# Optimization experiments

Hardware: AMD Instinct MI355X
Metric: run time of the kernel (lower is better)

Reference implementation:

```python
import jax, jax.numpy as jnp
import numpy as np

B, G, A = 16, 50, 81920          # batch, max_gt_num, anchor_num
T, P = 128, 64                   # train_anchors_num, max positives (T*positive_ratios)
NNEG = T - P                     # max negatives per image
BIG = 1e10


def setup_inputs():
    key = jax.random.key(0)
    k1, k2, k3, k4, k5, k6, k7 = jax.random.split(key, 7)
    # anchors: CTPN-style, fixed width 16, heights ~[11, 273]
    ay1 = jax.random.uniform(k1, (B, A)) * 960.0
    ax1 = jax.random.uniform(k2, (B, A)) * 1000.0
    ah = jax.random.uniform(k3, (B, A)) * 262.0 + 11.0
    anchors = jnp.stack([ay1, ax1, ay1 + ah, ax1 + 16.0], axis=-1)
    # gt boxes: 30 valid per image, rest padding (tag=0)
    gy1 = jax.random.uniform(k4, (B, G)) * 900.0
    gx1 = jax.random.uniform(k5, (B, G)) * 600.0
    gh = jax.random.uniform(k6, (B, G)) * 180.0 + 20.0
    gw = jax.random.uniform(k7, (B, G)) * 380.0 + 16.0
    tag = jnp.broadcast_to((jnp.arange(G) < 30).astype(jnp.float32), (B, G))
    boxes = jnp.stack([gy1, gx1, gy1 + gh, gx1 + gw], axis=-1) * tag[..., None]
    gt_boxes = jnp.concatenate([boxes, tag[..., None]], axis=-1)       # [B,G,5]
    gt_cls = jnp.stack([tag, tag], axis=-1)                            # [B,G,2] (class_id, tag)
    valid_anchors_indices = jnp.broadcast_to(jnp.arange(A, dtype=jnp.int32), (B, A))
    return {"gt_boxes": gt_boxes, "gt_cls": gt_cls, "anchors": anchors,
            "valid_anchors_indices": valid_anchors_indices}


def _compute_iou(gb, an):
    # gb [G,4], an [A,4] -> [G,A]
    iw = jnp.maximum(0.0, jnp.minimum(gb[:, None, 3], an[None, :, 3]) -
                     jnp.maximum(gb[:, None, 1], an[None, :, 1]))
    ih = jnp.maximum(0.0, jnp.minimum(gb[:, None, 2], an[None, :, 2]) -
                     jnp.maximum(gb[:, None, 0], an[None, :, 0]))
    inter = iw * ih
    area_g = (gb[:, 3] - gb[:, 1]) * (gb[:, 2] - gb[:, 0])
    area_a = (an[:, 3] - an[:, 1]) * (an[:, 2] - an[:, 0])
    return inter / (area_g[:, None] + area_a[None, :] - inter)


def _one_image(gt_boxes, gt_cls, anchors, valid_idx, key):
    gt_tag = gt_boxes[:, 4] > 0                       # [G] padding mask
    gb = gt_boxes[:, :4]
    gcls = gt_cls[:, 0]
    gt_num = jnp.sum(gt_tag.astype(jnp.float32))

    iou = _compute_iou(gb, anchors) * gt_tag[:, None].astype(jnp.float32)   # [G,A]
    gt_max_bool = (iou == jnp.max(iou, axis=1, keepdims=True)) & gt_tag[:, None]
    a_max = jnp.max(iou, axis=0, keepdims=True)
    a_thr = jnp.where(a_max >= 0.7, a_max, 1.0)
    pos_mat = (gt_max_bool | (iou == a_thr)) & gt_tag[:, None]              # [G,A]

    k1, k2 = jax.random.split(key)
    # --- positive sampling (random shuffle -> random-score top_k) ---
    flat = pos_mat.reshape(-1)
    score = jnp.where(flat, jax.random.uniform(k1, (G * A,)), -1.0)
    top_s, top_i = jax.lax.top_k(score, P)
    pos_valid = top_s >= 0.0                                               # [P]
    pos_num = jnp.sum(pos_valid.astype(jnp.int32))
    gt_i = top_i // A
    a_i = top_i % A
    pa = anchors[a_i]
    pg = gb[gt_i]
    pc = gcls[gt_i] * pos_valid
    h = pa[:, 2] - pa[:, 0]
    gt_h = jnp.where(pos_valid, pg[:, 2] - pg[:, 0], h)   # safe for padding slots
    dy = ((pg[:, 2] + pg[:, 0]) - (pa[:, 2] + pa[:, 0])) * 0.5 / h
    dh = jnp.log(gt_h / h)
    pd = jnp.stack([dy / 0.1, dh / 0.2], axis=1) * pos_valid[:, None]       # [P,2]

    # --- side anchors per gt ---
    x1b = jnp.broadcast_to(anchors[:, 1][None, :], (G, A))
    left_i = jnp.argmin(jnp.where(pos_mat, x1b, BIG), axis=1)
    right_i = jnp.argmax(jnp.where(pos_mat, x1b, -BIG), axis=1)
    la, ra = anchors[left_i], anchors[right_i]
    ld = (gb[:, 1] - (la[:, 3] + la[:, 1]) * 0.5) / (la[:, 3] - la[:, 1]) / 0.1
    rd = (gb[:, 3] - (ra[:, 3] + ra[:, 1]) * 0.5) / (ra[:, 3] - ra[:, 1]) / 0.1
    gtf = gt_tag.astype(jnp.float32)
    side_deltas = jnp.stack([ld * gtf, rd * gtf, gtf], axis=1)              # [G,3]
    gti = gt_tag.astype(jnp.int32)
    side_indices = jnp.stack([valid_idx[left_i] * gti, valid_idx[right_i] * gti, gti], axis=1)

    # --- negative sampling ---
    neg_bool = (jnp.max(iou, axis=0) < 0.5) & ~jnp.any(pos_mat, axis=0)
    nscore = jnp.where(neg_bool, jax.random.uniform(k2, (A,)), -1.0)
    ns, ni = jax.lax.top_k(nscore, NNEG)
    neg_avail = jnp.sum((ns >= 0.0).astype(jnp.int32))
    neg_num = jnp.minimum(jnp.minimum(NNEG, T - pos_num), neg_avail)

    # --- fixed-size assembly: slots [0,pos_num)=pos, [pos_num,pos_num+neg_num)=neg ---
    i = jnp.arange(T)
    is_pos = i < pos_num
    is_neg = (i >= pos_num) & (i < pos_num + neg_num)
    pi = jnp.clip(i, 0, P - 1)
    nj = jnp.clip(i - pos_num, 0, NNEG - 1)
    tagc = (is_pos | is_neg).astype(jnp.float32)
    deltas = jnp.concatenate([jnp.where(is_pos[:, None], pd[pi], 0.0), tagc[:, None]], axis=1)
    class_ids = jnp.stack([jnp.where(is_pos, pc[pi], 0.0), tagc], axis=1)
    idx_pos = valid_idx[a_i]                                                # [P]
    ind = jnp.where(is_pos, idx_pos[pi],
                    jnp.where(is_neg, ni[nj].astype(jnp.int32), 0))
    ind_tag = jnp.where(is_pos, 1, jnp.where(is_neg, -1, 0)).astype(jnp.int32)
    indices = jnp.stack([ind, ind_tag], axis=1)

    return (deltas, class_ids, indices, side_deltas, side_indices,
            gt_num, pos_num.astype(jnp.float32), neg_num.astype(jnp.float32))


def reference(gt_boxes, gt_cls, anchors, valid_anchors_indices):
    keys = jax.random.split(jax.random.key(42), B)
    return jax.vmap(_one_image)(gt_boxes, gt_cls, anchors, valid_anchors_indices, keys)
```

## Files before the change

kernel.cpp:

```cpp
#include <hip/hip_runtime.h>
#include <stdint.h>

namespace ct {
constexpr int B = 16, G = 50, A = 81920, T = 128;
constexpr int NB2 = 64;
constexpr int CH2 = A / (NB2 * 256);
constexpr int CAPP = 16384;
constexpr int CAPN = 16384;
constexpr int STG  = 7168;
constexpr int NX = 16, NY = 20, NCELL = NX * NY;
constexpr float NEG_T1 = 0.992f;

constexpr size_t O_DELTAS = 0;
constexpr size_t O_CLS = O_DELTAS + (size_t)B * T * 3;
constexpr size_t O_IND = O_CLS + (size_t)B * T * 2;
constexpr size_t O_SD  = O_IND + (size_t)B * T * 2;
constexpr size_t O_SI  = O_SD + (size_t)B * G * 3;
constexpr size_t O_GTN = O_SI + (size_t)B * G * 3;
constexpr size_t O_PN  = O_GTN + B;
constexpr size_t O_NN  = O_PN + B;

constexpr size_t W_KEYS  = 0;
constexpr size_t W_GTMAX = 256;
constexpr size_t W_LEFT  = 4096;
constexpr size_t W_RIGHT = 10496;
constexpr size_t W_CPOS  = 17408;
constexpr size_t W_CT1   = 18432;
constexpr size_t W_PNN   = 19456;
constexpr size_t W_BCNT  = 19584;
constexpr size_t W_PD0   = 24064;
constexpr size_t W_PD1   = W_PD0 + 4ull * B * 64;
constexpr size_t W_PC    = W_PD1 + 4ull * B * 64;
constexpr size_t W_IPF   = W_PC  + 4ull * B * 64;
constexpr size_t W_NI    = W_IPF + 4ull * B * 64;
constexpr size_t W_POSL  = W_NI  + 4ull * B * 64;
constexpr size_t W_NT1   = W_POSL + 8ull * B * CAPP;
constexpr size_t W_CMASK = W_NT1  + 8ull * B * CAPN;
}

struct U2 { uint32_t x, y; };

__device__ __forceinline__ U2 threefry(uint32_t k0, uint32_t k1, uint32_t x0, uint32_t x1) {
  uint32_t ks2 = k0 ^ k1 ^ 0x1BD11BDAu;
  x0 += k0; x1 += k1;
#define TFR(r) { x0 += x1; x1 = (x1 << (r)) | (x1 >> (32 - (r))); x1 ^= x0; }
  TFR(13) TFR(15) TFR(26) TFR(6)  x0 += k1;  x1 += ks2 + 1u;
  TFR(17) TFR(29) TFR(16) TFR(24) x0 += ks2; x1 += k0 + 2u;
  TFR(13) TFR(15) TFR(26) TFR(6)  x0 += k0;  x1 += k1 + 3u;
  TFR(17) TFR(29) TFR(16) TFR(24) x0 += k1;  x1 += ks2 + 4u;
  TFR(13) TFR(15) TFR(26) TFR(6)  x0 += ks2; x1 += k0 + 5u;
#undef TFR
  return {x0, x1};
}

__device__ __forceinline__ uint32_t rnd_bits(uint32_t ka, uint32_t kb, uint32_t idx) {
  U2 o = threefry(ka, kb, 0u, idx);
  return o.x ^ o.y;
}

__device__ __forceinline__ void iou_parts(float g0, float g1, float g2, float g3,
                                          float garea,
                                          float a0, float a1, float a2, float a3,
                                          float aarea, float& inter, float& denom) {
#pragma clang fp contract(off)
  float iw = fminf(g3, a3) - fmaxf(g1, a1);
  iw = fmaxf(0.0f, iw);
  float ih = fminf(g2, a2) - fmaxf(g0, a0);
  ih = fmaxf(0.0f, ih);
  inter = iw * ih;
  denom = (garea + aarea) - inter;
}

__device__ __forceinline__ void compact_gts(const float* gt_boxes, int b, int tid,
                                            float4* sgA, float* sgG, int* sgO,
                                            int* sn) {
  using namespace ct;
  int lane = tid & 63;
  if (tid < 64) {
    bool pred = false;
    float g0 = 0, g1 = 0, g2 = 0, g3 = 0;
    if (tid < G) {
      const float* gp = gt_boxes + ((size_t)b * G + tid) * 5;
      g0 = gp[0]; g1 = gp[1]; g2 = gp[2]; g3 = gp[3];
      pred = gp[4] > 0.0f;
    }
    unsigned long long mk = __ballot(pred);
    int slot = (int)__popcll(mk & ((1ull << lane) - 1ull));
    if (pred) {
      sgA[slot] = make_float4(g0, g1, g2, g3);
      sgG[slot] = (g3 - g1) * (g2 - g0);
      sgO[slot] = tid;
    }
    if (lane == 0) *sn = (int)__popcll(mk);
  }
}

__global__ __launch_bounds__(256) void k01_init(const float* __restrict__ gt_boxes,
                                                char* ws) {
  using namespace ct;
  __shared__ float4 sgA[64];
  __shared__ float  sgG[64];
  __shared__ int    sgO[64];
  __shared__ int    sn;
  int b = blockIdx.x, tid = threadIdx.x;
  if (tid == 0) {
    uint32_t* keys = (uint32_t*)(ws + W_KEYS);
    U2 kb = threefry(0u, 42u, 0u, (uint32_t)b);
    U2 s0 = threefry(kb.x, kb.y, 0u, 0u);
    U2 s1 = threefry(kb.x, kb.y, 0u, 1u);
    keys[b * 4 + 0] = s0.x; keys[b * 4 + 1] = s0.y;
    keys[b * 4 + 2] = s1.x; keys[b * 4 + 3] = s1.y;
    ((uint32_t*)(ws + W_CPOS))[b * 16] = 0u;
    ((uint32_t*)(ws + W_CT1))[b * 16] = 0u;
    ((uint32_t*)(ws + W_PNN))[b] = 0u;
    ((uint32_t*)(ws + W_PNN))[16 + b] = 0u;
  }
  if (tid >= 64 && tid < 64 + G) {
    int i = tid - 64;
    ((unsigned long long*)(ws + W_LEFT))[(size_t)b * G + i] = ~0ull;
    ((unsigned long long*)(ws + W_RIGHT))[(size_t)b * G + i] = 0ull;
    ((uint32_t*)(ws + W_GTMAX))[(size_t)b * G + i] = 0u;
  }
  compact_gts(gt_boxes, b, tid, sgA, sgG, sgO, &sn);
  __syncthreads();
  int ntag = sn;
  unsigned long long* cm = (unsigned long long*)(ws + W_CMASK) + (size_t)b * NCELL;
  for (int c = tid; c < NCELL; c += 256) {
    int cx = c & (NX - 1), cy = c >> 4;
    float x0 = cx * 64.0f, x1 = x0 + 64.0f;
    float y0 = cy * 64.0f, y1 = y0 + 64.0f;
    unsigned long long m = 0;
    for (int j = 0; j < ntag; ++j) {
      float4 g = sgA[j];
      if (g.y < x1 && g.w > x0 && g.x < y1 && g.z > y0) m |= 1ull << j;
    }
    cm[c] = m;
  }
}

__device__ __forceinline__ unsigned long long anchor_mask(const unsigned long long* sCM,
                                                          float4 an) {
  using namespace ct;
  int cx0 = min((int)an.y >> 6, NX - 1), cx1 = min((int)an.w >> 6, NX - 1);
  int cy0 = min((int)an.x >> 6, NY - 1), cy1 = min((int)an.z >> 6, NY - 1);
  unsigned long long mask = 0;
  for (int cy = cy0; cy <= cy1; ++cy)
    for (int cx = cx0; cx <= cx1; ++cx)
      mask |= sCM[cy * NX + cx];
  return mask;
}

__global__ __launch_bounds__(256) void k1b_gtmax(const float* __restrict__ anchors,
                                                 const float* __restrict__ gt_boxes,
                                                 char* ws) {
  using namespace ct;
  __shared__ float4 sgA[64];
  __shared__ float  sgG[64];
  __shared__ int    sgO[64];
  __shared__ int    sn;
  __shared__ uint32_t sGm[64];
  __shared__ unsigned long long sCM[NCELL];
  int b = blockIdx.y, tid = threadIdx.x;
  compact_gts(gt_boxes, b, tid, sgA, sgG, sgO, &sn);
  if (tid < 64) sGm[tid] = 0u;
  const unsigned long long* cm = (const unsigned long long*)(ws + W_CMASK) + (size_t)b * NCELL;
  for (int c = tid; c < NCELL; c += 256) sCM[c] = cm[c];
  __syncthreads();
  const float4* ap = (const float4*)(anchors + (size_t)b * A * 4);
  for (int c = 0; c < CH2; ++c) {
    int a = (blockIdx.x * CH2 + c) * 256 + tid;
    float4 an = ap[a];
    float aarea = (an.w - an.y) * (an.z - an.x);
    unsigned long long mask = anchor_mask(sCM, an);
    while (mask) {
      int j = (int)(__ffsll((long long)mask) - 1);
      mask &= mask - 1;
      float4 g = sgA[j];
      float inter, denom;
      iou_parts(g.x, g.y, g.z, g.w, sgG[j], an.x, an.y, an.z, an.w, aarea, inter, denom);
      float v = inter / denom;
      if (v > 0.0f) atomicMax(&sGm[j], __float_as_uint(v));
    }
  }
  __syncthreads();
  if (tid < sn && sGm[tid] != 0u)
    atomicMax((uint32_t*)(ws + W_GTMAX) + (size_t)b * G + sgO[tid], sGm[tid]);
}

__global__ __launch_bounds__(256) void k2_posneg(const float* __restrict__ anchors,
                                                 const float* __restrict__ gt_boxes,
                                                 char* ws) {
  using namespace ct;
  __shared__ float4 sgA[64];
  __shared__ float  sgG[64];
  __shared__ int    sgO[64];
  __shared__ float  sgM[64];
  __shared__ int    sn;
  __shared__ unsigned long long sCM[NCELL];
  __shared__ uint32_t sT1C[CH2];
  __shared__ uint32_t sWT1[CH2][4];
  __shared__ uint32_t sPfx[CH2];
  __shared__ uint32_t sNegW[4];
  __shared__ uint32_t sT1Base;
  int b = blockIdx.y, tid = threadIdx.x, lane = tid & 63, wid = tid >> 6;
  compact_gts(gt_boxes, b, tid, sgA, sgG, sgO, &sn);
  if (tid < CH2) sT1C[tid] = 0u;
  const unsigned long long* cm = (const unsigned long long*)(ws + W_CMASK) + (size_t)b * NCELL;
  for (int c = tid; c < NCELL; c += 256) sCM[c] = cm[c];
  __syncthreads();
  if (tid < sn)
    sgM[tid] = __uint_as_float(((const uint32_t*)(ws + W_GTMAX))[(size_t)b * G + sgO[tid]]);
  __syncthreads();

  const uint32_t* keys = (const uint32_t*)(ws + W_KEYS);
  uint32_t k1a = keys[b * 4 + 0], k1b = keys[b * 4 + 1];
  uint32_t k2a = keys[b * 4 + 2], k2b = keys[b * 4 + 3];
  unsigned long long* posl  = (unsigned long long*)(ws + W_POSL) + (size_t)b * CAPP;
  unsigned long long* negt1 = (unsigned long long*)(ws + W_NT1)  + (size_t)b * CAPN;
  unsigned long long* left  = (unsigned long long*)(ws + W_LEFT)  + (size_t)b * G;
  unsigned long long* right = (unsigned long long*)(ws + W_RIGHT) + (size_t)b * G;
  const float4* ap = (const float4*)(anchors + (size_t)b * A * 4);

  unsigned long long nkv[CH2];
  uint32_t offv[CH2];
  bool t1v[CH2];
  uint32_t negAcc = 0;

  for (int c = 0; c < CH2; ++c) {
    int a = (blockIdx.x * CH2 + c) * 256 + tid;
    float4 an = ap[a];
    float aarea = (an.w - an.y) * (an.z - an.x);
    unsigned long long mask = anchor_mask(sCM, an);

    float amax = 0.0f;
    unsigned long long mEq = 0, mMax = 0;
    unsigned long long t0 = mask;
    while (t0) {
      int j = (int)(__ffsll((long long)t0) - 1);
      t0 &= t0 - 1;
      float4 g = sgA[j];
      float inter, denom;
      iou_parts(g.x, g.y, g.z, g.w, sgG[j], an.x, an.y, an.z, an.w, aarea, inter, denom);
      float v = inter / denom;
      mEq |= (v == sgM[j]) ? (1ull << j) : 0ull;
      if (v > amax) { amax = v; mMax = 1ull << j; }
      else mMax |= (v == amax) ? (1ull << j) : 0ull;
    }
    unsigned long long pm = mEq | (amax >= 0.7f ? mMax : 0ull);

    if (__ballot(pm != 0)) {
      unsigned long long t = pm;
      while (t) {
        int j = (int)(__ffsll((long long)t) - 1);
        t &= t - 1;
        int g = sgO[j];
        uint32_t jg = (uint32_t)g * (uint32_t)A + (uint32_t)a;
        uint32_t m = rnd_bits(k1a, k1b, jg) >> 9;
        unsigned long long pk = ((unsigned long long)(m + 1u) << 32) | (0xFFFFFFFFu - jg);
        uint32_t idx = atomicAdd((uint32_t*)(ws + W_CPOS) + b * 16, 1u);
        if (idx < (uint32_t)CAPP) posl[idx] = pk;
        unsigned long long x1b = (unsigned long long)__float_as_uint(an.y);
        atomicMin(left + g,  (x1b << 32) | (uint32_t)a);
        atomicMax(right + g, (x1b << 32) | (0xFFFFFFFFu - (uint32_t)a));
      }
    }

    bool isneg = (amax < 0.5f) && (pm == 0);
    uint32_t m2 = rnd_bits(k2a, k2b, (uint32_t)a) >> 9;
    nkv[c] = ((unsigned long long)(m2 + 1u) << 32) | (0xFFFFFFFFu - (uint32_t)a);
    t1v[c] = isneg && ((float)m2 * (1.0f / 8388608.0f) >= NEG_T1);
    unsigned long long nm = __ballot(isneg);
    unsigned long long tm = __ballot(t1v[c]);
    offv[c] = (uint32_t)__popcll(tm & ((1ull << lane) - 1ull));
    if (lane == 0) {
      negAcc += (uint32_t)__popcll(nm);
      sWT1[c][wid] = atomicAdd(&sT1C[c], (uint32_t)__popcll(tm));
    }
  }
  if (lane == 0) sNegW[wid] = negAcc;
  __syncthreads();
  if (tid == 0) {
    uint32_t tot = 0;
    for (int c = 0; c < CH2; ++c) { sPfx[c] = tot; tot += sT1C[c]; }
    sT1Base = tot ? atomicAdd((uint32_t*)(ws + W_CT1) + b * 16, tot) : 0u;
    ((uint32_t*)(ws + W_BCNT))[b * NB2 + blockIdx.x] =
        sNegW[0] + sNegW[1] + sNegW[2] + sNegW[3];
  }
  __syncthreads();
  uint32_t base = sT1Base;
  for (int c = 0; c < CH2; ++c) {
    if (t1v[c]) {
      uint32_t idx = base + sPfx[c] + sWT1[c][wid] + offv[c];
      if (idx < (uint32_t)CAPN) negt1[idx] = nkv[c];
    }
  }
}

__device__ void select_top64(const unsigned long long* gsrc, int n,
                             unsigned long long* stage, unsigned long long* sel,
                             unsigned long long* wmax) {
  using namespace ct;
  int tid = threadIdx.x, lane = tid & 63, wid = tid >> 6;
  const unsigned long long* p = gsrc;
  if (n <= STG) {
    for (int i = tid; i < n; i += 256) stage[i] = gsrc[i];
    p = stage;
  }
  __syncthreads();
  unsigned long long prev = ~0ull;
  for (int k = 0; k < 64; ++k) {
    unsigned long long lm = 0;
    for (int i = tid; i < n; i += 256) {
      unsigned long long v = p[i];
      if (v < prev && v > lm) lm = v;
    }
#pragma unroll
    for (int off = 32; off >= 1; off >>= 1) {
      unsigned long long o = __shfl_xor(lm, off, 64);
      if (o > lm) lm = o;
    }
    if (lane == 0) wmax[wid] = lm;
    __syncthreads();
    if (tid == 0) {
      unsigned long long m = wmax[0];
      for (int w = 1; w < 4; ++w) if (wmax[w] > m) m = wmax[w];
      sel[k] = m;
    }
    __syncthreads();
    prev = sel[k];
  }
}

__device__ void bitonic_desc(const unsigned long long* gsrc, int n,
                             unsigned long long* stage) {
  int tid = threadIdx.x;
  int sz = 64;
  while (sz < n) sz <<= 1;
  for (int i = tid; i < sz; i += 256) stage[i] = (i < n) ? gsrc[i] : 0ull;
  __syncthreads();
  for (int k = 2; k <= sz; k <<= 1) {
    for (int j = k >> 1; j > 0; j >>= 1) {
      for (int i = tid; i < sz; i += 256) {
        int l = i ^ j;
        if (l > i) {
          unsigned long long a = stage[i], c = stage[l];
          bool dir = (i & k) == 0;
          if ((a < c) == dir) { stage[i] = c; stage[l] = a; }
        }
      }
      __syncthreads();
    }
  }
}

__global__ __launch_bounds__(256) void k34_select(const float* __restrict__ anchors,
                                                  const float* __restrict__ gt_boxes,
                                                  const float* __restrict__ gt_cls,
                                                  const int* __restrict__ vidx,
                                                  char* ws) {
  using namespace ct;
  __shared__ unsigned long long stage[STG];
  __shared__ unsigned long long sel[64];
  __shared__ unsigned long long wmax[4];
  __shared__ uint32_t scnt[4];
  int b = blockIdx.x, tid = threadIdx.x, lane = tid & 63, wid = tid >> 6;
  uint32_t* cnt_pnn = (uint32_t*)(ws + W_PNN);
  if (blockIdx.y == 0) {
    int n = (int)min(((const uint32_t*)(ws + W_CPOS))[b * 16], (uint32_t)CAPP);
    const unsigned long long* src = (const unsigned long long*)(ws + W_POSL) + (size_t)b * CAPP;
    if (n <= 2048) {
      bitonic_desc(src, n, stage);
      if (tid < 64) sel[tid] = stage[tid];
      __syncthreads();
    } else {
      select_top64(src, n, stage, sel, wmax);
    }
    int npos = n < 64 ? n : 64;
    if (tid == 0) cnt_pnn[b] = (uint32_t)npos;
    if (tid < 64) {
      float pd0 = 0.0f, pd1 = 0.0f, pcv = 0.0f, ipf = 0.0f;
      if (tid < npos) {
        uint32_t j = 0xFFFFFFFFu - (uint32_t)sel[tid];
        int g = j / (uint32_t)A, a = j % (uint32_t)A;
        const float* gp = gt_boxes + ((size_t)b * G + g) * 5;
        float4 an = *(const float4*)(anchors + ((size_t)b * A + a) * 4);
        float h = an.z - an.x;
        float gt_h = gp[2] - gp[0];
        float dy = (gp[2] + gp[0] - (an.z + an.x)) * 0.5f / h;
        float dh = logf(gt_h / h);
        pd0 = dy / 0.1f;
        pd1 = dh / 0.2f;
        pcv = gt_cls[((size_t)b * G + g) * 2];
        ipf = (float)vidx[(size_t)b * A + a];
      }
      ((float*)(ws + W_PD0))[b * 64 + tid] = pd0;
      ((float*)(ws + W_PD1))[b * 64 + tid] = pd1;
      ((float*)(ws + W_PC ))[b * 64 + tid] = pcv;
      ((float*)(ws + W_IPF))[b * 64 + tid] = ipf;
    }
  } else {
    const uint32_t* bc = (const uint32_t*)(ws + W_BCNT) + (size_t)b * NB2;
    uint32_t callv = 0;
    for (int i = tid; i < NB2; i += 256) callv += bc[i];
#pragma unroll
    for (int off = 32; off >= 1; off >>= 1) callv += __shfl_xor(callv, off, 64);
    if (lane == 0) scnt[wid] = callv;
    __syncthreads();
    int call = (int)(scnt[0] + scnt[1] + scnt[2] + scnt[3]);
    int c1 = (int)min(((const uint32_t*)(ws + W_CT1))[b * 16], (uint32_t)CAPN);
    if (c1 <= 2048) {
      bitonic_desc((const unsigned long long*)(ws + W_NT1) + (size_t)b * CAPN, c1, stage);
      if (tid < 64) sel[tid] = stage[tid];
      __syncthreads();
    } else {
      select_top64((const unsigned long long*)(ws + W_NT1) + (size_t)b * CAPN, c1,
                   stage, sel, wmax);
    }
    int nn = call < 64 ? call : 64;
    if (nn > c1) nn = c1;
    if (tid == 0) cnt_pnn[16 + b] = (uint32_t)nn;
    if (tid < 64) {
      int v = 0;
      if (tid < nn) v = (int)(0xFFFFFFFFu - (uint32_t)sel[tid]);
      ((int*)(ws + W_NI))[b * 64 + tid] = v;
    }
  }
}

__global__ __launch_bounds__(256) void k5_out(const float* __restrict__ anchors,
                                              const float* __restrict__ gt_boxes,
                                              const int* __restrict__ vidx,
                                              char* ws, float* __restrict__ out) {
  using namespace ct;
  int b = blockIdx.x, tid = threadIdx.x;
  const uint32_t* cnt_pnn = (const uint32_t*)(ws + W_PNN);
  int pn = (int)cnt_pnn[b];
  int nn = (int)cnt_pnn[16 + b];
  if (tid < T) {
    int t = tid;
    bool ispos = t < pn;
    bool isneg = (t >= pn) && (t < pn + nn);
    float tagc = (ispos || isneg) ? 1.0f : 0.0f;
    int tp = t < 63 ? t : 63;
    float d0 = ispos ? ((const float*)(ws + W_PD0))[b * 64 + tp] : 0.0f;
    float d1 = ispos ? ((const float*)(ws + W_PD1))[b * 64 + tp] : 0.0f;
    out[O_DELTAS + ((size_t)b * T + t) * 3 + 0] = d0;
    out[O_DELTAS + ((size_t)b * T + t) * 3 + 1] = d1;
    out[O_DELTAS + ((size_t)b * T + t) * 3 + 2] = tagc;
    float c0 = ispos ? ((const float*)(ws + W_PC))[b * 64 + tp] : 0.0f;
    out[O_CLS + ((size_t)b * T + t) * 2 + 0] = c0;
    out[O_CLS + ((size_t)b * T + t) * 2 + 1] = tagc;
    float iv = 0.0f, itag = 0.0f;
    if (ispos) {
      iv = ((const float*)(ws + W_IPF))[b * 64 + tp];
      itag = 1.0f;
    } else if (isneg) {
      int nj = t - pn; nj = nj < 63 ? nj : 63;
      iv = (float)((const int*)(ws + W_NI))[b * 64 + nj];
      itag = -1.0f;
    }
    out[O_IND + ((size_t)b * T + t) * 2 + 0] = iv;
    out[O_IND + ((size_t)b * T + t) * 2 + 1] = itag;
  }
  if (tid >= 128 && tid < 128 + G) {
    int g = tid - 128;
    const float* gp = gt_boxes + ((size_t)b * G + g) * 5;
    float tag = gp[4] > 0.0f ? 1.0f : 0.0f;
    float sd0 = 0.0f, sd1 = 0.0f, si0 = 0.0f, si1 = 0.0f;
    if (tag > 0.0f) {
      unsigned long long lp = ((const unsigned long long*)(ws + W_LEFT))[(size_t)b * G + g];
      unsigned long long rp = ((const unsigned long long*)(ws + W_RIGHT))[(size_t)b * G + g];
      int al = (int)(uint32_t)lp;
      int ar = (int)(0xFFFFFFFFu - (uint32_t)rp);
      float4 la = *(const float4*)(anchors + ((size_t)b * A + al) * 4);
      float4 ra = *(const float4*)(anchors + ((size_t)b * A + ar) * 4);
      sd0 = (gp[1] - (la.w + la.y) * 0.5f) / (la.w - la.y) / 0.1f;
      sd1 = (gp[3] - (ra.w + ra.y) * 0.5f) / (ra.w - ra.y) / 0.1f;
      si0 = (float)vidx[(size_t)b * A + al];
      si1 = (float)vidx[(size_t)b * A + ar];
    }
    out[O_SD + ((size_t)b * G + g) * 3 + 0] = sd0;
    out[O_SD + ((size_t)b * G + g) * 3 + 1] = sd1;
    out[O_SD + ((size_t)b * G + g) * 3 + 2] = tag;
    out[O_SI + ((size_t)b * G + g) * 3 + 0] = si0;
    out[O_SI + ((size_t)b * G + g) * 3 + 1] = si1;
    out[O_SI + ((size_t)b * G + g) * 3 + 2] = tag;
  }
  if (tid == 190) {
    float s = 0.0f;
    for (int g = 0; g < G; ++g)
      s += (gt_boxes[((size_t)b * G + g) * 5 + 4] > 0.0f) ? 1.0f : 0.0f;
    out[O_GTN + b] = s;
  }
  if (tid == 191) out[O_PN + b] = (float)pn;
  if (tid == 192) out[O_NN + b] = (float)nn;
}

extern "C" void kernel_launch(void* const* d_in, const int* in_sizes, int n_in,
                              void* d_out, int out_size, void* d_ws, size_t ws_size,
                              hipStream_t stream) {
  using namespace ct;
  (void)in_sizes; (void)n_in; (void)out_size; (void)ws_size;
  const float* gt_boxes = (const float*)d_in[0];
  const float* gt_cls   = (const float*)d_in[1];
  const float* anchors  = (const float*)d_in[2];
  const int*   vidx     = (const int*)d_in[3];
  float* out = (float*)d_out;
  char* ws = (char*)d_ws;

  k01_init<<<dim3(B), dim3(256), 0, stream>>>(gt_boxes, ws);
  k1b_gtmax<<<dim3(NB2, B), dim3(256), 0, stream>>>(anchors, gt_boxes, ws);
  k2_posneg<<<dim3(NB2, B), dim3(256), 0, stream>>>(anchors, gt_boxes, ws);
  k34_select<<<dim3(B, 2), dim3(256), 0, stream>>>(anchors, gt_boxes, gt_cls, vidx, ws);
  k5_out<<<dim3(B), dim3(256), 0, stream>>>(anchors, gt_boxes, vidx, ws, out);
}
```

Baseline: 164.9 us.

## Fuse init, select and output kernels; build cell masks in shared memory

Removes the init kernel by moving workspace clearing to memset calls, and has each gtmax and posneg block rebuild the grid cell masks and RNG keys in shared memory instead of reading them from global memory. The two selection halves and the output kernel are merged into one per-image kernel that keeps intermediates in shared memory. This cuts kernel launches and global round trips. In exchange, the positive and negative selections now run one after the other in 16 blocks instead of 32 parallel blocks, the cell mask work is repeated in every block, and the staging buffer shrinks to 2048 entries.

```diff
diff --git a/kernel.cpp b/kernel.cpp
--- a/kernel.cpp
+++ b/kernel.cpp
@@ -7,7 +7,7 @@
 constexpr int CH2 = A / (NB2 * 256);
 constexpr int CAPP = 16384;
 constexpr int CAPN = 16384;
-constexpr int STG  = 7168;
+constexpr int STG  = 2048;
 constexpr int NX = 16, NY = 20, NCELL = NX * NY;
 constexpr float NEG_T1 = 0.992f;
 
@@ -20,22 +20,16 @@
 constexpr size_t O_PN  = O_GTN + B;
 constexpr size_t O_NN  = O_PN + B;
 
-constexpr size_t W_KEYS  = 0;
-constexpr size_t W_GTMAX = 256;
-constexpr size_t W_LEFT  = 4096;
-constexpr size_t W_RIGHT = 10496;
-constexpr size_t W_CPOS  = 17408;
-constexpr size_t W_CT1   = 18432;
-constexpr size_t W_PNN   = 19456;
-constexpr size_t W_BCNT  = 19584;
-constexpr size_t W_PD0   = 24064;
-constexpr size_t W_PD1   = W_PD0 + 4ull * B * 64;
-constexpr size_t W_PC    = W_PD1 + 4ull * B * 64;
-constexpr size_t W_IPF   = W_PC  + 4ull * B * 64;
-constexpr size_t W_NI    = W_IPF + 4ull * B * 64;
-constexpr size_t W_POSL  = W_NI  + 4ull * B * 64;
+constexpr size_t W_LEFT  = 0;
+constexpr size_t W_GTMAX = 8192;
+constexpr size_t W_RIGHT = 11392;
+constexpr size_t W_CPOS  = 17792;
+constexpr size_t W_CT1   = 18816;
+constexpr size_t W_ZERO0 = W_GTMAX;
+constexpr size_t W_ZSIZE = 19840 - W_GTMAX;
+constexpr size_t W_BCNT  = 19840;
+constexpr size_t W_POSL  = 24064;
 constexpr size_t W_NT1   = W_POSL + 8ull * B * CAPP;
-constexpr size_t W_CMASK = W_NT1  + 8ull * B * CAPN;
 }
 
 struct U2 { uint32_t x, y; };
@@ -95,36 +89,9 @@
   }
 }
 
-__global__ __launch_bounds__(256) void k01_init(const float* __restrict__ gt_boxes,
-                                                char* ws) {
-  using namespace ct;
-  __shared__ float4 sgA[64];
-  __shared__ float  sgG[64];
-  __shared__ int    sgO[64];
-  __shared__ int    sn;
-  int b = blockIdx.x, tid = threadIdx.x;
-  if (tid == 0) {
-    uint32_t* keys = (uint32_t*)(ws + W_KEYS);
-    U2 kb = threefry(0u, 42u, 0u, (uint32_t)b);
-    U2 s0 = threefry(kb.x, kb.y, 0u, 0u);
-    U2 s1 = threefry(kb.x, kb.y, 0u, 1u);
-    keys[b * 4 + 0] = s0.x; keys[b * 4 + 1] = s0.y;
-    keys[b * 4 + 2] = s1.x; keys[b * 4 + 3] = s1.y;
-    ((uint32_t*)(ws + W_CPOS))[b * 16] = 0u;
-    ((uint32_t*)(ws + W_CT1))[b * 16] = 0u;
-    ((uint32_t*)(ws + W_PNN))[b] = 0u;
-    ((uint32_t*)(ws + W_PNN))[16 + b] = 0u;
-  }
-  if (tid >= 64 && tid < 64 + G) {
-    int i = tid - 64;
-    ((unsigned long long*)(ws + W_LEFT))[(size_t)b * G + i] = ~0ull;
-    ((unsigned long long*)(ws + W_RIGHT))[(size_t)b * G + i] = 0ull;
-    ((uint32_t*)(ws + W_GTMAX))[(size_t)b * G + i] = 0u;
-  }
-  compact_gts(gt_boxes, b, tid, sgA, sgG, sgO, &sn);
-  __syncthreads();
-  int ntag = sn;
-  unsigned long long* cm = (unsigned long long*)(ws + W_CMASK) + (size_t)b * NCELL;
+__device__ __forceinline__ void build_cellmask(const float4* sgA, int ntag, int tid,
+                                               unsigned long long* sCM) {
+  using namespace ct;
   for (int c = tid; c < NCELL; c += 256) {
     int cx = c & (NX - 1), cy = c >> 4;
     float x0 = cx * 64.0f, x1 = x0 + 64.0f;
@@ -134,7 +101,7 @@
       float4 g = sgA[j];
       if (g.y < x1 && g.w > x0 && g.x < y1 && g.z > y0) m |= 1ull << j;
     }
-    cm[c] = m;
+    sCM[c] = m;
   }
 }
 
@@ -163,8 +130,8 @@
   int b = blockIdx.y, tid = threadIdx.x;
   compact_gts(gt_boxes, b, tid, sgA, sgG, sgO, &sn);
   if (tid < 64) sGm[tid] = 0u;
-  const unsigned long long* cm = (const unsigned long long*)(ws + W_CMASK) + (size_t)b * NCELL;
-  for (int c = tid; c < NCELL; c += 256) sCM[c] = cm[c];
+  __syncthreads();
+  build_cellmask(sgA, sn, tid, sCM);
   __syncthreads();
   const float4* ap = (const float4*)(anchors + (size_t)b * A * 4);
   for (int c = 0; c < CH2; ++c) {
@@ -197,6 +164,7 @@
   __shared__ float  sgM[64];
   __shared__ int    sn;
   __shared__ unsigned long long sCM[NCELL];
+  __shared__ uint32_t sK[4];
   __shared__ uint32_t sT1C[CH2];
   __shared__ uint32_t sWT1[CH2][4];
   __shared__ uint32_t sPfx[CH2];
@@ -205,16 +173,24 @@
   int b = blockIdx.y, tid = threadIdx.x, lane = tid & 63, wid = tid >> 6;
   compact_gts(gt_boxes, b, tid, sgA, sgG, sgO, &sn);
   if (tid < CH2) sT1C[tid] = 0u;
-  const unsigned long long* cm = (const unsigned long long*)(ws + W_CMASK) + (size_t)b * NCELL;
-  for (int c = tid; c < NCELL; c += 256) sCM[c] = cm[c];
+  if (tid == 64 || (tid == 0 && blockDim.x == 64)) {}
+  if (tid == 65 % 256) {}
+  if (tid == 66 % 256) {}
+  if (tid == 0) {
+    U2 kb = threefry(0u, 42u, 0u, (uint32_t)b);
+    U2 s0 = threefry(kb.x, kb.y, 0u, 0u);
+    U2 s1 = threefry(kb.x, kb.y, 0u, 1u);
+    sK[0] = s0.x; sK[1] = s0.y;
+    sK[2] = s1.x; sK[3] = s1.y;
+  }
+  __syncthreads();
+  build_cellmask(sgA, sn, tid, sCM);
   __syncthreads();
   if (tid < sn)
     sgM[tid] = __uint_as_float(((const uint32_t*)(ws + W_GTMAX))[(size_t)b * G + sgO[tid]]);
   __syncthreads();
 
-  const uint32_t* keys = (const uint32_t*)(ws + W_KEYS);
-  uint32_t k1a = keys[b * 4 + 0], k1b = keys[b * 4 + 1];
-  uint32_t k2a = keys[b * 4 + 2], k2b = keys[b * 4 + 3];
+  uint32_t k1a = sK[0], k1b = sK[1], k2a = sK[2], k2b = sK[3];
   unsigned long long* posl  = (unsigned long long*)(ws + W_POSL) + (size_t)b * CAPP;
   unsigned long long* negt1 = (unsigned long long*)(ws + W_NT1)  + (size_t)b * CAPN;
   unsigned long long* left  = (unsigned long long*)(ws + W_LEFT)  + (size_t)b * G;
@@ -353,22 +329,25 @@
   }
 }
 
-__global__ __launch_bounds__(256) void k34_select(const float* __restrict__ anchors,
-                                                  const float* __restrict__ gt_boxes,
-                                                  const float* __restrict__ gt_cls,
-                                                  const int* __restrict__ vidx,
-                                                  char* ws) {
+__global__ __launch_bounds__(256) void k345_out(const float* __restrict__ anchors,
+                                                const float* __restrict__ gt_boxes,
+                                                const float* __restrict__ gt_cls,
+                                                const int* __restrict__ vidx,
+                                                char* ws, float* __restrict__ out) {
   using namespace ct;
   __shared__ unsigned long long stage[STG];
   __shared__ unsigned long long sel[64];
   __shared__ unsigned long long wmax[4];
   __shared__ uint32_t scnt[4];
+  __shared__ float sPD0[64], sPD1[64], sPC[64], sIPF[64];
+  __shared__ int sNI[64];
+  __shared__ int sPn, sNn;
   int b = blockIdx.x, tid = threadIdx.x, lane = tid & 63, wid = tid >> 6;
-  uint32_t* cnt_pnn = (uint32_t*)(ws + W_PNN);
-  if (blockIdx.y == 0) {
+
+  {
     int n = (int)min(((const uint32_t*)(ws + W_CPOS))[b * 16], (uint32_t)CAPP);
     const unsigned long long* src = (const unsigned long long*)(ws + W_POSL) + (size_t)b * CAPP;
-    if (n <= 2048) {
+    if (n <= STG) {
       bitonic_desc(src, n, stage);
       if (tid < 64) sel[tid] = stage[tid];
       __syncthreads();
@@ -376,7 +355,7 @@
       select_top64(src, n, stage, sel, wmax);
     }
     int npos = n < 64 ? n : 64;
-    if (tid == 0) cnt_pnn[b] = (uint32_t)npos;
+    if (tid == 0) sPn = npos;
     if (tid < 64) {
       float pd0 = 0.0f, pd1 = 0.0f, pcv = 0.0f, ipf = 0.0f;
       if (tid < npos) {
@@ -393,12 +372,12 @@
         pcv = gt_cls[((size_t)b * G + g) * 2];
         ipf = (float)vidx[(size_t)b * A + a];
       }
-      ((float*)(ws + W_PD0))[b * 64 + tid] = pd0;
-      ((float*)(ws + W_PD1))[b * 64 + tid] = pd1;
-      ((float*)(ws + W_PC ))[b * 64 + tid] = pcv;
-      ((float*)(ws + W_IPF))[b * 64 + tid] = ipf;
-    }
-  } else {
+      sPD0[tid] = pd0; sPD1[tid] = pd1; sPC[tid] = pcv; sIPF[tid] = ipf;
+    }
+  }
+  __syncthreads();
+
+  {
     const uint32_t* bc = (const uint32_t*)(ws + W_BCNT) + (size_t)b * NB2;
     uint32_t callv = 0;
     for (int i = tid; i < NB2; i += 256) callv += bc[i];
@@ -408,7 +387,7 @@
     __syncthreads();
     int call = (int)(scnt[0] + scnt[1] + scnt[2] + scnt[3]);
     int c1 = (int)min(((const uint32_t*)(ws + W_CT1))[b * 16], (uint32_t)CAPN);
-    if (c1 <= 2048) {
+    if (c1 <= STG) {
       bitonic_desc((const unsigned long long*)(ws + W_NT1) + (size_t)b * CAPN, c1, stage);
       if (tid < 64) sel[tid] = stage[tid];
       __syncthreads();
@@ -418,46 +397,34 @@
     }
     int nn = call < 64 ? call : 64;
     if (nn > c1) nn = c1;
-    if (tid == 0) cnt_pnn[16 + b] = (uint32_t)nn;
+    if (tid == 0) sNn = nn;
     if (tid < 64) {
       int v = 0;
       if (tid < nn) v = (int)(0xFFFFFFFFu - (uint32_t)sel[tid]);
-      ((int*)(ws + W_NI))[b * 64 + tid] = v;
-    }
-  }
-}
-
-__global__ __launch_bounds__(256) void k5_out(const float* __restrict__ anchors,
-                                              const float* __restrict__ gt_boxes,
-                                              const int* __restrict__ vidx,
-                                              char* ws, float* __restrict__ out) {
-  using namespace ct;
-  int b = blockIdx.x, tid = threadIdx.x;
-  const uint32_t* cnt_pnn = (const uint32_t*)(ws + W_PNN);
-  int pn = (int)cnt_pnn[b];
-  int nn = (int)cnt_pnn[16 + b];
+      sNI[tid] = v;
+    }
+  }
+  __syncthreads();
+
+  int pn = sPn, nn = sNn;
   if (tid < T) {
     int t = tid;
     bool ispos = t < pn;
     bool isneg = (t >= pn) && (t < pn + nn);
     float tagc = (ispos || isneg) ? 1.0f : 0.0f;
     int tp = t < 63 ? t : 63;
-    float d0 = ispos ? ((const float*)(ws + W_PD0))[b * 64 + tp] : 0.0f;
-    float d1 = ispos ? ((const float*)(ws + W_PD1))[b * 64 + tp] : 0.0f;
+    float d0 = ispos ? sPD0[tp] : 0.0f;
+    float d1 = ispos ? sPD1[tp] : 0.0f;
     out[O_DELTAS + ((size_t)b * T + t) * 3 + 0] = d0;
     out[O_DELTAS + ((size_t)b * T + t) * 3 + 1] = d1;
     out[O_DELTAS + ((size_t)b * T + t) * 3 + 2] = tagc;
-    float c0 = ispos ? ((const float*)(ws + W_PC))[b * 64 + tp] : 0.0f;
-    out[O_CLS + ((size_t)b * T + t) * 2 + 0] = c0;
+    out[O_CLS + ((size_t)b * T + t) * 2 + 0] = ispos ? sPC[tp] : 0.0f;
     out[O_CLS + ((size_t)b * T + t) * 2 + 1] = tagc;
     float iv = 0.0f, itag = 0.0f;
-    if (ispos) {
-      iv = ((const float*)(ws + W_IPF))[b * 64 + tp];
-      itag = 1.0f;
-    } else if (isneg) {
+    if (ispos) { iv = sIPF[tp]; itag = 1.0f; }
+    else if (isneg) {
       int nj = t - pn; nj = nj < 63 ? nj : 63;
-      iv = (float)((const int*)(ws + W_NI))[b * 64 + nj];
-      itag = -1.0f;
+      iv = (float)sNI[nj]; itag = -1.0f;
     }
     out[O_IND + ((size_t)b * T + t) * 2 + 0] = iv;
     out[O_IND + ((size_t)b * T + t) * 2 + 1] = itag;
@@ -508,9 +475,9 @@
   float* out = (float*)d_out;
   char* ws = (char*)d_ws;
 
-  k01_init<<<dim3(B), dim3(256), 0, stream>>>(gt_boxes, ws);
+  hipMemsetAsync(ws + W_LEFT, 0xFF, 8ull * B * G, stream);
+  hipMemsetAsync(ws + W_ZERO0, 0, W_ZSIZE, stream);
   k1b_gtmax<<<dim3(NB2, B), dim3(256), 0, stream>>>(anchors, gt_boxes, ws);
   k2_posneg<<<dim3(NB2, B), dim3(256), 0, stream>>>(anchors, gt_boxes, ws);
-  k34_select<<<dim3(B, 2), dim3(256), 0, stream>>>(anchors, gt_boxes, gt_cls, vidx, ws);
-  k5_out<<<dim3(B), dim3(256), 0, stream>>>(anchors, gt_boxes, vidx, ws, out);
-}
+  k345_out<<<dim3(B), dim3(256), 0, stream>>>(anchors, gt_boxes, gt_cls, vidx, ws, out);
+}
```

Measured after the change: 178.4 us. 1.08x slower.
